# Performance work log

Hardware: AMD Instinct MI355X
Metric: run time of the kernel (lower is better)

The kernel has to match this reference:

```python
import jax, jax.numpy as jnp
import numpy as np

N = 50000      # num nodes
E = 800000     # num edges (avg degree 16)
D_IN = 128     # input feature dim
H = 128        # hidden dim
RD = 32        # relation embedding dim
L = 2          # num layers
R = 16         # num relations


def setup_inputs() -> dict:
    key = jax.random.key(0)
    ks = jax.random.split(key, 16)
    f32 = jnp.float32
    def lin(k, out_d, in_d):
        return jax.random.normal(k, (out_d, in_d), dtype=f32) * (1.0 / np.sqrt(in_d))
    return {
        "x": jax.random.normal(ks[0], (N, D_IN), dtype=f32),
        "in_W": lin(ks[1], H, D_IN),
        "in_b": jnp.zeros((H,), f32),
        # per-layer stacked params [L, ...]
        "rel_emb": jax.random.normal(ks[2], (L, R, RD), dtype=f32) * 0.02,
        "msg_W": jax.random.normal(ks[3], (L, H, H + RD), dtype=f32) * (1.0 / np.sqrt(H + RD)),
        "msg_b": jnp.zeros((L, H), f32),
        "self_W": jax.random.normal(ks[4], (L, H, H), dtype=f32) * (1.0 / np.sqrt(H)),
        "self_b": jnp.zeros((L, H), f32),
        "neigh_W": jax.random.normal(ks[5], (L, H, H), dtype=f32) * (1.0 / np.sqrt(H)),
        "neigh_b": jnp.zeros((L, H), f32),
        "edge_src": jax.random.randint(ks[6], (E,), 0, N),
        "edge_dst": jax.random.randint(ks[7], (E,), 0, N),
        "rel_ids": jax.random.randint(ks[8], (E,), 0, R),
    }


def reference(x, in_W, in_b, rel_emb, msg_W, msg_b, self_W, self_b,
              neigh_W, neigh_b, edge_src, edge_dst, rel_ids):
    # input projection (dropout is identity at eval)
    h = x @ in_W.T + in_b
    ones_e = jnp.ones((edge_dst.shape[0], 1), h.dtype)
    deg = jax.ops.segment_sum(ones_e, edge_dst, num_segments=N)   # [N,1]
    deg = jnp.maximum(deg, 1.0)
    for l in range(L):
        rel = rel_emb[l][rel_ids]                                  # [E,RD] gather
        msg_in = jnp.concatenate([h[edge_src], rel], axis=-1)      # [E,H+RD]
        msg = msg_in @ msg_W[l].T + msg_b[l]                       # [E,H]
        agg = jax.ops.segment_sum(msg, edge_dst, num_segments=N) / deg  # mean agg
        h = jax.nn.relu(h @ self_W[l].T + self_b[l] + agg @ neigh_W[l].T + neigh_b[l])
    return h
```

## Files before the change

kernel.cpp:

```cpp
#include <hip/hip_runtime.h>
#include <hip/hip_bf16.h>

#define NN 50000
#define EE 800000
#define DH 128
#define RDIM 32
#define RR 16
#define HRD 160
#define HSW 272
#define SCAN_B ((NN + 255) / 256)

typedef __attribute__((ext_vector_type(8))) short bf16x8;
typedef __attribute__((ext_vector_type(4))) float f32x4;

__device__ __forceinline__ ushort f2b(float v) {
    uint u = __float_as_uint(v);
    return (ushort)((u + 0x7fffu + ((u >> 16) & 1u)) >> 16);
}
__device__ __forceinline__ float b2f(ushort b) { return __uint_as_float(((uint)b) << 16); }


__global__ __launch_bounds__(256) void k_count(const int* __restrict__ dst,
                                               const int* __restrict__ rel,
                                               int* deg, int* cnt) {
    int e = blockIdx.x * 256 + threadIdx.x;
    if (e < EE) {
        int d = dst[e];
        atomicAdd(&deg[d], 1);
        atomicAdd(&cnt[d * RR + rel[e]], 1);
    }
}

__global__ __launch_bounds__(256) void k_scan_part(const int* __restrict__ deg,
                                                   int* rp, int* bsum) {
    __shared__ int s[256];
    int tid = threadIdx.x;
    int i = blockIdx.x * 256 + tid;
    int v = (i < NN) ? deg[i] : 0;
    s[tid] = v;
    __syncthreads();
    for (int off = 1; off < 256; off <<= 1) {
        int t = (tid >= off) ? s[tid - off] : 0;
        __syncthreads();
        s[tid] += t;
        __syncthreads();
    }
    if (i < NN) rp[i] = s[tid] - v;
    if (tid == 255) bsum[blockIdx.x] = s[255];
}

__global__ __launch_bounds__(256) void k_scan_bsum(const int* __restrict__ bsum, int* boff) {
    __shared__ int s[256];
    int tid = threadIdx.x;
    int v = (tid < SCAN_B) ? bsum[tid] : 0;
    s[tid] = v;
    __syncthreads();
    for (int off = 1; off < 256; off <<= 1) {
        int t = (tid >= off) ? s[tid - off] : 0;
        __syncthreads();
        s[tid] += t;
        __syncthreads();
    }
    boff[tid] = s[tid] - v;
}

__global__ __launch_bounds__(256) void k_scan_add(const int* __restrict__ boff,
                                                  int* rp, int* fill) {
    int i = blockIdx.x * 256 + threadIdx.x;
    if (i < NN) {
        int v = rp[i] + boff[blockIdx.x];
        rp[i] = v;
        fill[i] = v;
    }
    if (i == 0) rp[NN] = EE;
}

__global__ __launch_bounds__(256) void k_fill(const int* __restrict__ src,
                                              const int* __restrict__ dst,
                                              int* fill, int* col) {
    int e = blockIdx.x * 256 + threadIdx.x;
    if (e < EE) {
        int p = atomicAdd(&fill[dst[e]], 1);
        col[p] = src[e];
    }
}


__global__ __launch_bounds__(256) void k_prep_inWb(const float* __restrict__ w,
                                                   ushort* __restrict__ o) {
    int i = blockIdx.x * 256 + threadIdx.x;
    o[i] = f2b(w[i]);
}

__global__ __launch_bounds__(256) void k_prep_msgWb(const float* __restrict__ msgW,
                                                    const float* __restrict__ relE,
                                                    ushort* __restrict__ B1) {
    int t = threadIdx.x;
    int l = t >> 7, f = t & 127;
    const float* mw = msgW + (size_t)l * DH * HRD + f * HRD;
    ushort* out = B1 + (size_t)l * DH * 144 + f * 144;
    for (int k = 0; k < DH; ++k) out[k] = f2b(mw[k]);
    for (int r = 0; r < RR; ++r) {
        float acc = 0.f;
        for (int c = 0; c < RDIM; ++c)
            acc += relE[l * RR * RDIM + r * RDIM + c] * mw[DH + c];
        out[DH + r] = f2b(acc);
    }
}

__global__ __launch_bounds__(256) void k_prep_wc2b(const float* __restrict__ selfW,
                                                   const float* __restrict__ neighW,
                                                   ushort* __restrict__ o) {
    int idx = blockIdx.x * 256 + threadIdx.x;
    int l = idx >> 15, rem = idx & 32767;
    int f = rem >> 8, k = rem & 255;
    float v = (k < DH) ? selfW[(size_t)l * DH * DH + f * DH + k]
                       : neighW[(size_t)l * DH * DH + f * DH + (k - DH)];
    o[idx] = f2b(v);
}

__global__ __launch_bounds__(256) void k_cntbf(const int* __restrict__ cnt,
                                               ushort* __restrict__ hs) {
    int idx = blockIdx.x * 256 + threadIdx.x;
    if (idx < NN * RR) {
        int n = idx >> 4, r = idx & 15;
        hs[(size_t)n * HSW + 256 + r] = f2b((float)cnt[idx]);
    }
}

__global__ __launch_bounds__(256) void k_seg(ushort* __restrict__ hs,
                                             const int* __restrict__ rp,
                                             const int* __restrict__ col) {
    int wid = threadIdx.x >> 6, lane = threadIdx.x & 63;
    int n = blockIdx.x * 4 + wid;
    if (n >= NN) return;
    int beg = rp[n], end = rp[n + 1];
    float ax = 0.f, ay = 0.f;
    for (int j0 = beg; j0 < end; j0 += 64) {
        int myc = (j0 + lane < end) ? col[j0 + lane] : 0;
        int m = min(64, end - j0);
        for (int jj = 0; jj < m; ++jj) {
            int sidx = __shfl(myc, jj, 64);
            uint v = *(const uint*)(hs + (size_t)sidx * HSW + lane * 2);
            ax += b2f((ushort)(v & 0xffffu));
            ay += b2f((ushort)(v >> 16));
        }
    }
    uint packed = ((uint)f2b(ay) << 16) | (uint)f2b(ax);
    *(uint*)(hs + (size_t)n * HSW + 128 + lane * 2) = packed;
}

template <int K, int EPI, int AMODE>
__global__ __launch_bounds__(256) void k_mm(const void* __restrict__ Araw,
                                            const ushort* __restrict__ B,
                                            const float* __restrict__ bias1,
                                            const float* __restrict__ bias2,
                                            const int* __restrict__ deg,
                                            ushort* __restrict__ hs,
                                            float* __restrict__ outf) {
    constexpr int KC = (K == 256) ? 128 : K;
    constexpr int NCH = K / KC;
    constexpr int KP = KC + 8;
    __shared__ ushort A_s[64][KP];
    __shared__ ushort B_s[128][KP];
    __shared__ int deg_s[64];
    int t = threadIdx.x;
    int n0 = blockIdx.x * 64;
    int lane = t & 63, wid = t >> 6;
    int wm = wid >> 1, wn = wid & 1;

    if (EPI == 1 && t < 64) {
        int node = n0 + t;
        deg_s[t] = (node < NN) ? deg[node] : 1;
    }

    f32x4 acc[2][4];
    #pragma unroll
    for (int mt = 0; mt < 2; ++mt)
        #pragma unroll
        for (int nt = 0; nt < 4; ++nt) acc[mt][nt] = (f32x4)0.0f;

    for (int ch = 0; ch < NCH; ++ch) {
        int kc0 = ch * KC;
        if (AMODE == 0) {
            const float4* x4 = (const float4*)Araw;
            for (int idx = t; idx < 64 * (KC / 4); idx += 256) {
                int r = idx / (KC / 4), c = idx % (KC / 4);
                int node = min(n0 + r, NN - 1);
                float4 v = x4[(size_t)node * 32 + c];
                ushort* dst = &A_s[r][c * 4];
                dst[0] = f2b(v.x); dst[1] = f2b(v.y);
                dst[2] = f2b(v.z); dst[3] = f2b(v.w);
            }
        } else {
            const ushort* Ab = (const ushort*)Araw;
            for (int idx = t; idx < 64 * (KC / 8); idx += 256) {
                int r = idx / (KC / 8), c = idx % (KC / 8);
                int node = min(n0 + r, NN - 1);
                *(uint4*)&A_s[r][c * 8] =
                    *(const uint4*)(Ab + (size_t)node * HSW + kc0 + c * 8);
            }
        }
        for (int idx = t; idx < 128 * (KC / 8); idx += 256) {
            int r = idx / (KC / 8), c = idx % (KC / 8);
            *(uint4*)&B_s[r][c * 8] =
                *(const uint4*)(B + (size_t)r * K + kc0 + c * 8);
        }
        __syncthreads();

        #pragma unroll
        for (int ks = 0; ks < KC / 32; ++ks) {
            int k0 = ks * 32 + (lane >> 4) * 8;
            bf16x8 af[2], bfr[4];
            #pragma unroll
            for (int mt = 0; mt < 2; ++mt)
                af[mt] = *(const bf16x8*)&A_s[wm * 32 + mt * 16 + (lane & 15)][k0];
            #pragma unroll
            for (int nt = 0; nt < 4; ++nt)
                bfr[nt] = *(const bf16x8*)&B_s[wn * 64 + nt * 16 + (lane & 15)][k0];
            #pragma unroll
            for (int mt = 0; mt < 2; ++mt)
                #pragma unroll
                for (int nt = 0; nt < 4; ++nt)
                    acc[mt][nt] = __builtin_amdgcn_mfma_f32_16x16x32_bf16(
                        af[mt], bfr[nt], acc[mt][nt], 0, 0, 0);
        }
        if (ch + 1 < NCH) __syncthreads();
    }

    int fbase = wn * 64;
    #pragma unroll
    for (int mt = 0; mt < 2; ++mt) {
        #pragma unroll
        for (int rg = 0; rg < 4; ++rg) {
            int nl = wm * 32 + mt * 16 + ((lane >> 4) << 2) + rg;
            int node = n0 + nl;
            if (node >= NN) continue;
            #pragma unroll
            for (int nt = 0; nt < 4; ++nt) {
                int f = fbase + nt * 16 + (lane & 15);
                float v = acc[mt][nt][rg];
                if (EPI == 0) {
                    hs[(size_t)node * HSW + f] = f2b(v + bias1[f]);
                } else if (EPI == 1) {
                    int d = deg_s[nl];
                    float o = v * (1.f / (float)max(d, 1)) + ((d > 0) ? bias1[f] : 0.f);
                    hs[(size_t)node * HSW + 128 + f] = f2b(o);
                } else {
                    float o = fmaxf(v + bias1[f] + bias2[f], 0.f);
                    if (EPI == 2) hs[(size_t)node * HSW + f] = f2b(o);
                    else          outf[(size_t)node * DH + f] = o;
                }
            }
        }
    }
}

extern "C" void kernel_launch(void* const* d_in, const int* in_sizes, int n_in,
                              void* d_out, int out_size, void* d_ws, size_t ws_size,
                              hipStream_t stream) {
    const float* x      = (const float*)d_in[0];
    const float* in_W   = (const float*)d_in[1];
    const float* in_b   = (const float*)d_in[2];
    const float* rel_e  = (const float*)d_in[3];
    const float* msg_W  = (const float*)d_in[4];
    const float* msg_b  = (const float*)d_in[5];
    const float* self_b = (const float*)d_in[7];
    const float* self_W = (const float*)d_in[6];
    const float* neigh_W= (const float*)d_in[8];
    const float* neigh_b= (const float*)d_in[9];
    const int* e_src    = (const int*)d_in[10];
    const int* e_dst    = (const int*)d_in[11];
    const int* r_ids    = (const int*)d_in[12];

    char* ws = (char*)d_ws;
    size_t off = 0;
    ushort* HS   = (ushort*)(ws + off); off += (size_t)NN * HSW * 2;
    ushort* inWb = (ushort*)(ws + off); off += (size_t)DH * DH * 2;
    ushort* B1   = (ushort*)(ws + off); off += 2 * (size_t)DH * 144 * 2;
    ushort* Wc2b = (ushort*)(ws + off); off += 2 * (size_t)DH * 256 * 2;
    int* deg  = (int*)(ws + off);
    int* cnt  = deg + NN;
    int* rp   = cnt + (size_t)NN * RR;
    int* fill = rp + NN + 1;
    int* bsum = fill + NN;
    int* boff = bsum + 256;
    int* col  = boff + 256;

    hipMemsetAsync(deg, 0, sizeof(int) * (NN + (size_t)NN * RR), stream);

    k_count<<<(EE + 255) / 256, 256, 0, stream>>>(e_dst, r_ids, deg, cnt);
    k_scan_part<<<SCAN_B, 256, 0, stream>>>(deg, rp, bsum);
    k_scan_bsum<<<1, 256, 0, stream>>>(bsum, boff);
    k_scan_add<<<SCAN_B, 256, 0, stream>>>(boff, rp, fill);
    k_fill<<<(EE + 255) / 256, 256, 0, stream>>>(e_src, e_dst, fill, col);

    k_cntbf<<<(NN * RR + 255) / 256, 256, 0, stream>>>(cnt, HS);
    k_prep_inWb<<<64, 256, 0, stream>>>(in_W, inWb);
    k_prep_msgWb<<<1, 256, 0, stream>>>(msg_W, rel_e, B1);
    k_prep_wc2b<<<256, 256, 0, stream>>>(self_W, neigh_W, Wc2b);

    const int GB = (NN + 63) / 64;
    k_mm<128, 0, 0><<<GB, 256, 0, stream>>>(x, inWb, in_b, nullptr, nullptr, HS, nullptr);

    for (int l = 0; l < 2; ++l) {
        k_seg<<<(NN + 3) / 4, 256, 0, stream>>>(HS, rp, col);
        k_mm<144, 1, 1><<<GB, 256, 0, stream>>>(HS + 128, B1 + (size_t)l * DH * 144,
                                                msg_b + l * DH, nullptr, deg, HS, nullptr);
        if (l == 0)
            k_mm<256, 2, 2><<<GB, 256, 0, stream>>>(HS, Wc2b, self_b, neigh_b,
                                                    nullptr, HS, nullptr);
        else
            k_mm<256, 3, 2><<<GB, 256, 0, stream>>>(HS, Wc2b + (size_t)DH * 256,
                                                    self_b + DH, neigh_b + DH,
                                                    nullptr, HS, (float*)d_out);
    }
}
```

Before: 436.6 us.

## Fold relation term into segment gather and build CSR without fill atomics

```diff
diff --git a/kernel.cpp b/kernel.cpp
--- a/kernel.cpp
+++ b/kernel.cpp
@@ -7,7 +7,7 @@
 #define RDIM 32
 #define RR 16
 #define HRD 160
-#define HSW 272
+#define HSW 384
 #define SCAN_B ((NN + 255) / 256)
 
 typedef __attribute__((ext_vector_type(8))) short bf16x8;
@@ -19,16 +19,10 @@
 }
 __device__ __forceinline__ float b2f(ushort b) { return __uint_as_float(((uint)b) << 16); }
 
-
 __global__ __launch_bounds__(256) void k_count(const int* __restrict__ dst,
-                                               const int* __restrict__ rel,
-                                               int* deg, int* cnt) {
+                                               int* deg, int* ord) {
     int e = blockIdx.x * 256 + threadIdx.x;
-    if (e < EE) {
-        int d = dst[e];
-        atomicAdd(&deg[d], 1);
-        atomicAdd(&cnt[d * RR + rel[e]], 1);
-    }
+    if (e < EE) ord[e] = atomicAdd(&deg[dst[e]], 1);
 }
 
 __global__ __launch_bounds__(256) void k_scan_part(const int* __restrict__ deg,
@@ -64,24 +58,22 @@
     boff[tid] = s[tid] - v;
 }
 
-__global__ __launch_bounds__(256) void k_scan_add(const int* __restrict__ boff,
-                                                  int* rp, int* fill) {
+__global__ __launch_bounds__(256) void k_scan_add(const int* __restrict__ boff, int* rp) {
     int i = blockIdx.x * 256 + threadIdx.x;
-    if (i < NN) {
-        int v = rp[i] + boff[blockIdx.x];
-        rp[i] = v;
-        fill[i] = v;
-    }
+    if (i < NN) rp[i] += boff[blockIdx.x];
     if (i == 0) rp[NN] = EE;
 }
 
 __global__ __launch_bounds__(256) void k_fill(const int* __restrict__ src,
                                               const int* __restrict__ dst,
-                                              int* fill, int* col) {
+                                              const int* __restrict__ rel,
+                                              const int* __restrict__ ord,
+                                              const int* __restrict__ rp,
+                                              int* __restrict__ col) {
     int e = blockIdx.x * 256 + threadIdx.x;
     if (e < EE) {
-        int p = atomicAdd(&fill[dst[e]], 1);
-        col[p] = src[e];
+        int p = rp[dst[e]] + ord[e];
+        col[p] = src[e] | (rel[e] << 16);
     }
 }
 
@@ -94,17 +86,18 @@
 
 __global__ __launch_bounds__(256) void k_prep_msgWb(const float* __restrict__ msgW,
                                                     const float* __restrict__ relE,
-                                                    ushort* __restrict__ B1) {
+                                                    ushort* __restrict__ B1,
+                                                    float* __restrict__ RMf32) {
     int t = threadIdx.x;
     int l = t >> 7, f = t & 127;
     const float* mw = msgW + (size_t)l * DH * HRD + f * HRD;
-    ushort* out = B1 + (size_t)l * DH * 144 + f * 144;
+    ushort* out = B1 + ((size_t)l * DH + f) * DH;
     for (int k = 0; k < DH; ++k) out[k] = f2b(mw[k]);
     for (int r = 0; r < RR; ++r) {
         float acc = 0.f;
         for (int c = 0; c < RDIM; ++c)
             acc += relE[l * RR * RDIM + r * RDIM + c] * mw[DH + c];
-        out[DH + r] = f2b(acc);
+        RMf32[(size_t)l * RR * DH + r * DH + f] = acc;
     }
 }
 
@@ -119,35 +112,38 @@
     o[idx] = f2b(v);
 }
 
-__global__ __launch_bounds__(256) void k_cntbf(const int* __restrict__ cnt,
-                                               ushort* __restrict__ hs) {
-    int idx = blockIdx.x * 256 + threadIdx.x;
-    if (idx < NN * RR) {
-        int n = idx >> 4, r = idx & 15;
-        hs[(size_t)n * HSW + 256 + r] = f2b((float)cnt[idx]);
-    }
-}
-
 __global__ __launch_bounds__(256) void k_seg(ushort* __restrict__ hs,
                                              const int* __restrict__ rp,
-                                             const int* __restrict__ col) {
-    int wid = threadIdx.x >> 6, lane = threadIdx.x & 63;
+                                             const int* __restrict__ col,
+                                             const float* __restrict__ RM) {
+    __shared__ float RM_s[RR * DH];
+    int t = threadIdx.x;
+    for (int i = t; i < RR * DH; i += 256) RM_s[i] = RM[i];
+    __syncthreads();
+    int wid = t >> 6, lane = t & 63;
     int n = blockIdx.x * 4 + wid;
     if (n >= NN) return;
     int beg = rp[n], end = rp[n + 1];
-    float ax = 0.f, ay = 0.f;
+    float ax = 0.f, ay = 0.f, rx = 0.f, ry = 0.f;
+    const float* rm0 = RM_s + lane * 2;
     for (int j0 = beg; j0 < end; j0 += 64) {
         int myc = (j0 + lane < end) ? col[j0 + lane] : 0;
         int m = min(64, end - j0);
         for (int jj = 0; jj < m; ++jj) {
-            int sidx = __shfl(myc, jj, 64);
+            int packed = __shfl(myc, jj, 64);
+            int sidx = packed & 0xffff;
+            int rel = packed >> 16;
             uint v = *(const uint*)(hs + (size_t)sidx * HSW + lane * 2);
             ax += b2f((ushort)(v & 0xffffu));
             ay += b2f((ushort)(v >> 16));
-        }
-    }
-    uint packed = ((uint)f2b(ay) << 16) | (uint)f2b(ax);
-    *(uint*)(hs + (size_t)n * HSW + 128 + lane * 2) = packed;
+            rx += rm0[rel * DH];
+            ry += rm0[rel * DH + 1];
+        }
+    }
+    uint ps = ((uint)f2b(ay) << 16) | (uint)f2b(ax);
+    uint pr = ((uint)f2b(ry) << 16) | (uint)f2b(rx);
+    *(uint*)(hs + (size_t)n * HSW + 128 + lane * 2) = ps;
+    *(uint*)(hs + (size_t)n * HSW + 256 + lane * 2) = pr;
 }
 
 template <int K, int EPI, int AMODE>
@@ -188,9 +184,9 @@
                 int r = idx / (KC / 4), c = idx % (KC / 4);
                 int node = min(n0 + r, NN - 1);
                 float4 v = x4[(size_t)node * 32 + c];
-                ushort* dst = &A_s[r][c * 4];
-                dst[0] = f2b(v.x); dst[1] = f2b(v.y);
-                dst[2] = f2b(v.z); dst[3] = f2b(v.w);
+                ushort* dstp = &A_s[r][c * 4];
+                dstp[0] = f2b(v.x); dstp[1] = f2b(v.y);
+                dstp[2] = f2b(v.z); dstp[3] = f2b(v.w);
             }
         } else {
             const ushort* Ab = (const ushort*)Araw;
@@ -244,7 +240,9 @@
                     hs[(size_t)node * HSW + f] = f2b(v + bias1[f]);
                 } else if (EPI == 1) {
                     int d = deg_s[nl];
-                    float o = v * (1.f / (float)max(d, 1)) + ((d > 0) ? bias1[f] : 0.f);
+                    float rmacc = b2f(hs[(size_t)node * HSW + 256 + f]);
+                    float o = (v + rmacc) * (1.f / (float)max(d, 1))
+                              + ((d > 0) ? bias1[f] : 0.f);
                     hs[(size_t)node * HSW + 128 + f] = f2b(o);
                 } else {
                     float o = fmaxf(v + bias1[f] + bias2[f], 0.f);
@@ -265,8 +263,8 @@
     const float* rel_e  = (const float*)d_in[3];
     const float* msg_W  = (const float*)d_in[4];
     const float* msg_b  = (const float*)d_in[5];
+    const float* self_W = (const float*)d_in[6];
     const float* self_b = (const float*)d_in[7];
-    const float* self_W = (const float*)d_in[6];
     const float* neigh_W= (const float*)d_in[8];
     const float* neigh_b= (const float*)d_in[9];
     const int* e_src    = (const int*)d_in[10];
@@ -277,41 +275,40 @@
     size_t off = 0;
     ushort* HS   = (ushort*)(ws + off); off += (size_t)NN * HSW * 2;
     ushort* inWb = (ushort*)(ws + off); off += (size_t)DH * DH * 2;
-    ushort* B1   = (ushort*)(ws + off); off += 2 * (size_t)DH * 144 * 2;
+    ushort* B1   = (ushort*)(ws + off); off += 2 * (size_t)DH * DH * 2;
     ushort* Wc2b = (ushort*)(ws + off); off += 2 * (size_t)DH * 256 * 2;
+    float*  RMf  = (float*)(ws + off);  off += 2 * (size_t)RR * DH * 4;
     int* deg  = (int*)(ws + off);
-    int* cnt  = deg + NN;
-    int* rp   = cnt + (size_t)NN * RR;
-    int* fill = rp + NN + 1;
-    int* bsum = fill + NN;
+    int* rp   = deg + NN;
+    int* bsum = rp + NN + 1;
     int* boff = bsum + 256;
-    int* col  = boff + 256;
-
-    hipMemsetAsync(deg, 0, sizeof(int) * (NN + (size_t)NN * RR), stream);
-
-    k_count<<<(EE + 255) / 256, 256, 0, stream>>>(e_dst, r_ids, deg, cnt);
+    int* ord  = boff + 256;
+    int* col  = ord + EE;
+
+    hipMemsetAsync(deg, 0, sizeof(int) * NN, stream);
+
+    k_count<<<(EE + 255) / 256, 256, 0, stream>>>(e_dst, deg, ord);
     k_scan_part<<<SCAN_B, 256, 0, stream>>>(deg, rp, bsum);
     k_scan_bsum<<<1, 256, 0, stream>>>(bsum, boff);
-    k_scan_add<<<SCAN_B, 256, 0, stream>>>(boff, rp, fill);
-    k_fill<<<(EE + 255) / 256, 256, 0, stream>>>(e_src, e_dst, fill, col);
-
-    k_cntbf<<<(NN * RR + 255) / 256, 256, 0, stream>>>(cnt, HS);
+    k_scan_add<<<SCAN_B, 256, 0, stream>>>(boff, rp);
+    k_fill<<<(EE + 255) / 256, 256, 0, stream>>>(e_src, e_dst, r_ids, ord, rp, col);
+
     k_prep_inWb<<<64, 256, 0, stream>>>(in_W, inWb);
-    k_prep_msgWb<<<1, 256, 0, stream>>>(msg_W, rel_e, B1);
+    k_prep_msgWb<<<1, 256, 0, stream>>>(msg_W, rel_e, B1, RMf);
     k_prep_wc2b<<<256, 256, 0, stream>>>(self_W, neigh_W, Wc2b);
 
     const int GB = (NN + 63) / 64;
     k_mm<128, 0, 0><<<GB, 256, 0, stream>>>(x, inWb, in_b, nullptr, nullptr, HS, nullptr);
 
     for (int l = 0; l < 2; ++l) {
-        k_seg<<<(NN + 3) / 4, 256, 0, stream>>>(HS, rp, col);
-        k_mm<144, 1, 1><<<GB, 256, 0, stream>>>(HS + 128, B1 + (size_t)l * DH * 144,
+        k_seg<<<(NN + 3) / 4, 256, 0, stream>>>(HS, rp, col, RMf + (size_t)l * RR * DH);
+        k_mm<128, 1, 1><<<GB, 256, 0, stream>>>(HS + 128, B1 + (size_t)l * DH * DH,
                                                 msg_b + l * DH, nullptr, deg, HS, nullptr);
         if (l == 0)
-            k_mm<256, 2, 2><<<GB, 256, 0, stream>>>(HS, Wc2b, self_b, neigh_b,
+            k_mm<256, 2, 1><<<GB, 256, 0, stream>>>(HS, Wc2b, self_b, neigh_b,
                                                     nullptr, HS, nullptr);
         else
-            k_mm<256, 3, 2><<<GB, 256, 0, stream>>>(HS, Wc2b + (size_t)DH * 256,
+            k_mm<256, 3, 1><<<GB, 256, 0, stream>>>(HS, Wc2b + (size_t)DH * 256,
                                                     self_b + DH, neigh_b + DH,
                                                     nullptr, HS, (float*)d_out);
     }
```

After: 395.3 us. 9.5% less time.
